# Optimization experiments

Measured on AMD Instinct MI355X. Metric: run time of the kernel, lower is better.

The kernel has to match this reference:

```python
import jax, jax.numpy as jnp
import numpy as np

OUT_FEATURES = 4096
IN_FEATURES = 4096
BATCH = 2048
NNZ = 1_600_000


def setup_inputs() -> dict:
    key = jax.random.key(0)
    k1, k2, k3, k4, k5 = jax.random.split(key, 5)
    rows = jax.random.randint(k1, (NNZ,), 0, OUT_FEATURES, dtype=jnp.int32)
    cols = jax.random.randint(k2, (NNZ,), 0, IN_FEATURES, dtype=jnp.int32)
    values = jax.random.normal(k3, (NNZ,), dtype=jnp.float32) * 0.02
    bias = jax.random.normal(k4, (OUT_FEATURES, 1), dtype=jnp.float32) * 0.02
    inp = jax.random.normal(k5, (IN_FEATURES, BATCH), dtype=jnp.float32)
    return {"inp": inp, "values": values, "bias": bias, "rows": rows, "cols": cols}


def reference(inp, values, bias, rows, cols):
    # Sparse COO addmm: out = bias + W @ inp, W sparse [OUT, IN].
    # Scatter-add the COO triplets into a dense weight (sums duplicates,
    # matching coalesced-COO spmm semantics), then one dense GEMM.
    W = jnp.zeros((OUT_FEATURES, IN_FEATURES), dtype=values.dtype).at[rows, cols].add(values)
    return W @ inp + bias  # [OUT, BATCH], bias [OUT,1] broadcasts over batch
```

## Files before the change

### kernel.cpp

```cpp
#include <hip/hip_runtime.h>
#include <stdint.h>

#define OUTF 4096
#define INF  4096
#define NBAT 2048
#define BM 128
#define BN 128
#define BK 32

typedef __attribute__((ext_vector_type(8))) short bf16x8;
typedef __attribute__((ext_vector_type(4))) float f32x4;
typedef __attribute__((ext_vector_type(4))) unsigned int u32x4;

typedef const __attribute__((address_space(1))) uint8_t* gptr_t;
typedef __attribute__((address_space(3))) uint8_t* lptr_t;

__device__ __forceinline__ uint32_t f2bf(float f) {
  uint32_t u = __builtin_bit_cast(uint32_t, f);
  return (u + 0x7FFFu + ((u >> 16) & 1u)) >> 16;
}

__global__ void zeroW_kernel(uint4* __restrict__ W) {
  W[(size_t)blockIdx.x * 256 + threadIdx.x] = make_uint4(0u, 0u, 0u, 0u);
}

__global__ void scatter_kernel(const float* __restrict__ vals,
                               const int* __restrict__ rows,
                               const int* __restrict__ cols,
                               float* __restrict__ W, int nnz) {
  int i = blockIdx.x * blockDim.x + threadIdx.x;
  if (i < nnz) atomicAdd(&W[(size_t)rows[i] * INF + cols[i]], vals[i]);
}

__global__ void packW_kernel(uint32_t* __restrict__ W) {
  size_t i = ((size_t)blockIdx.x * 256 + threadIdx.x) * 4;
  uint4 p = *(const uint4*)(W + i);
  uint32_t o[4];
  uint32_t w[4] = {p.x, p.y, p.z, p.w};
#pragma unroll
  for (int j = 0; j < 4; ++j) {
    float f = __builtin_bit_cast(float, w[j]);
    uint32_t hi = f2bf(f);
    float fhi = __builtin_bit_cast(float, hi << 16);
    uint32_t lo = f2bf(f - fhi);
    o[j] = (hi << 16) | lo;
  }
  *(uint4*)(W + i) = make_uint4(o[0], o[1], o[2], o[3]);
}

__global__ void packX_kernel(const float* __restrict__ X,
                             uint16_t* __restrict__ Xh,
                             uint16_t* __restrict__ Xl) {
  __shared__ float t[32][33];
  int n0 = blockIdx.x * 32, k0 = blockIdx.y * 32;
  int tx = threadIdx.x, ty = threadIdx.y;
#pragma unroll
  for (int j = 0; j < 4; ++j)
    t[ty + j * 8][tx] = X[(size_t)(k0 + ty + j * 8) * NBAT + n0 + tx];
  __syncthreads();
#pragma unroll
  for (int j = 0; j < 4; ++j) {
    int n = n0 + ty + j * 8, k = k0 + tx;
    float f = t[tx][ty + j * 8];
    uint32_t hi = f2bf(f);
    float fhi = __builtin_bit_cast(float, hi << 16);
    uint32_t lo = f2bf(f - fhi);
    Xh[(size_t)n * INF + k] = (uint16_t)hi;
    Xl[(size_t)n * INF + k] = (uint16_t)lo;
  }
}

__global__ __launch_bounds__(256, 2) void gemm_kernel(
    const uint32_t* __restrict__ Wp,
    const uint16_t* __restrict__ Xh,
    const uint16_t* __restrict__ Xl,
    const float* __restrict__ bias,
    float* __restrict__ out) {
  __shared__ __align__(16) uint8_t lds[32768];
  uint8_t* la = lds;
  uint8_t* lb = lds + 16384;

  const unsigned tid = threadIdx.x;
  const unsigned lane = tid & 63, wid = tid >> 6;
  const unsigned wr = wid >> 1, wc = wid & 1;

  unsigned newid = (blockIdx.x & 7) * 64 + (blockIdx.x >> 3);
  const unsigned bm = newid & 31, bn = newid >> 5;

  const uint8_t* aSrc[4];
  const uint8_t* bSrc[4];
#pragma unroll
  for (int i = 0; i < 4; ++i) {
    unsigned d = i * 4096 + tid * 16;
    unsigned row = d >> 7;
    unsigned ch = (d >> 4) & 7;
    unsigned sc = ch ^ (row & 7);
    aSrc[i] = (const uint8_t*)Wp + (size_t)(bm * BM + row) * (INF * 4) + sc * 16;
    const uint16_t* base = (sc & 4) ? Xl : Xh;
    bSrc[i] = (const uint8_t*)(base + (size_t)(bn * BN + row) * INF + (sc & 3) * 8);
  }

  const unsigned kg = lane >> 4, lr = lane & 15;
  unsigned aOff[4][2], bOffH[4], bOffL[4];
#pragma unroll
  for (int mi = 0; mi < 4; ++mi) {
    unsigned row = wr * 64 + mi * 16 + lr;
    aOff[mi][0] = row * 128 + (((kg * 2 + 0) ^ (row & 7)) * 16);
    aOff[mi][1] = row * 128 + (((kg * 2 + 1) ^ (row & 7)) * 16);
  }
#pragma unroll
  for (int ni = 0; ni < 4; ++ni) {
    unsigned col = wc * 64 + ni * 16 + lr;
    bOffH[ni] = col * 128 + (((0 + kg) ^ (col & 7)) * 16);
    bOffL[ni] = col * 128 + (((4 + kg) ^ (col & 7)) * 16);
  }

  f32x4 acc[4][4] = {};

  for (unsigned kt = 0; kt < INF / BK; ++kt) {
#pragma unroll
    for (int i = 0; i < 4; ++i) {
      __builtin_amdgcn_global_load_lds((gptr_t)(aSrc[i] + (size_t)kt * 128),
                                       (lptr_t)(la + i * 4096 + wid * 1024), 16, 0, 0);
      __builtin_amdgcn_global_load_lds((gptr_t)(bSrc[i] + (size_t)kt * 64),
                                       (lptr_t)(lb + i * 4096 + wid * 1024), 16, 0, 0);
    }
    __syncthreads();

    bf16x8 ah[4], al[4], bh[4], bl[4];
#pragma unroll
    for (int mi = 0; mi < 4; ++mi) {
      uint4 p0 = *(const uint4*)(la + aOff[mi][0]);
      uint4 p1 = *(const uint4*)(la + aOff[mi][1]);
      u32x4 h, l;
      h[0] = (p0.x >> 16) | (p0.y & 0xFFFF0000u);  l[0] = (p0.x & 0xFFFFu) | (p0.y << 16);
      h[1] = (p0.z >> 16) | (p0.w & 0xFFFF0000u);  l[1] = (p0.z & 0xFFFFu) | (p0.w << 16);
      h[2] = (p1.x >> 16) | (p1.y & 0xFFFF0000u);  l[2] = (p1.x & 0xFFFFu) | (p1.y << 16);
      h[3] = (p1.z >> 16) | (p1.w & 0xFFFF0000u);  l[3] = (p1.z & 0xFFFFu) | (p1.w << 16);
      ah[mi] = __builtin_bit_cast(bf16x8, h);
      al[mi] = __builtin_bit_cast(bf16x8, l);
    }
#pragma unroll
    for (int ni = 0; ni < 4; ++ni) {
      bh[ni] = *(const bf16x8*)(lb + bOffH[ni]);
      bl[ni] = *(const bf16x8*)(lb + bOffL[ni]);
    }
#pragma unroll
    for (int mi = 0; mi < 4; ++mi)
#pragma unroll
      for (int ni = 0; ni < 4; ++ni) {
        acc[mi][ni] = __builtin_amdgcn_mfma_f32_16x16x32_bf16(ah[mi], bh[ni], acc[mi][ni], 0, 0, 0);
        acc[mi][ni] = __builtin_amdgcn_mfma_f32_16x16x32_bf16(ah[mi], bl[ni], acc[mi][ni], 0, 0, 0);
        acc[mi][ni] = __builtin_amdgcn_mfma_f32_16x16x32_bf16(al[mi], bh[ni], acc[mi][ni], 0, 0, 0);
      }
    __syncthreads();
  }

  const unsigned lq = lane >> 4;
#pragma unroll
  for (int mi = 0; mi < 4; ++mi) {
    unsigned row0 = bm * BM + wr * 64 + mi * 16 + lq * 4;
#pragma unroll
    for (int ni = 0; ni < 4; ++ni) {
      unsigned col = bn * BN + wc * 64 + ni * 16 + lr;
#pragma unroll
      for (int r = 0; r < 4; ++r)
        out[(size_t)(row0 + r) * NBAT + col] = acc[mi][ni][r] + bias[row0 + r];
    }
  }
}

extern "C" void kernel_launch(void* const* d_in, const int* in_sizes, int n_in,
                              void* d_out, int out_size, void* d_ws, size_t ws_size,
                              hipStream_t stream) {
  const float* inp    = (const float*)d_in[0];
  const float* values = (const float*)d_in[1];
  const float* bias   = (const float*)d_in[2];
  const int*   rows   = (const int*)d_in[3];
  const int*   cols   = (const int*)d_in[4];
  const int nnz = in_sizes[1];
  float* out = (float*)d_out;

  uint8_t* ws = (uint8_t*)d_ws;
  float*    W  = (float*)ws;
  uint16_t* Xh = (uint16_t*)(ws + (64u << 20));
  uint16_t* Xl = (uint16_t*)(ws + (80u << 20));

  zeroW_kernel<<<(OUTF * (size_t)INF * 4) / (256 * 16), 256, 0, stream>>>((uint4*)W);
  scatter_kernel<<<(nnz + 255) / 256, 256, 0, stream>>>(values, rows, cols, W, nnz);
  packW_kernel<<<(OUTF * (size_t)INF / 4) / 256, 256, 0, stream>>>((uint32_t*)W);
  packX_kernel<<<dim3(NBAT / 32, INF / 32), dim3(32, 8), 0, stream>>>(inp, Xh, Xl);
  gemm_kernel<<<(OUTF / BM) * (NBAT / BN), 256, 0, stream>>>(
      (const uint32_t*)W, Xh, Xl, bias, out);
}
```

Baseline: 391.0 us.

## Fuse zero/packX, drop packW, split fp32 W in GEMM with pipelined split-K

Merges W zeroing and X packing into one launch and removes the separate W packing pass. The GEMM now reads raw fp32 W and splits it into bf16 hi/lo in registers. The GEMM moves to 128-thread blocks where two waves split K, with a double-buffered LDS pipeline, 32x32x16 MFMAs, and a reduction plus coalesced bias store through LDS. This removes a full 64MB read-write pass over W and kernel launch overhead, at the cost of more A-tile traffic and in-loop unpack ALU work. The lo part is now truncated instead of rounded, and there is only one block per CU.

Measured after the change: 1.390 ms. 3.55x slower.

```diff
diff --git a/kernel.cpp b/kernel.cpp
--- a/kernel.cpp
+++ b/kernel.cpp
@@ -4,14 +4,12 @@
 #define OUTF 4096
 #define INF  4096
 #define NBAT 2048
-#define BM 128
-#define BN 128
-#define BK 32
+#define T_STEPS 128
 
 typedef __attribute__((ext_vector_type(8))) short bf16x8;
+typedef __attribute__((ext_vector_type(16))) float f32x16;
 typedef __attribute__((ext_vector_type(4))) float f32x4;
 typedef __attribute__((ext_vector_type(4))) unsigned int u32x4;
-
 typedef const __attribute__((address_space(1))) uint8_t* gptr_t;
 typedef __attribute__((address_space(3))) uint8_t* lptr_t;
 
@@ -20,40 +18,28 @@
   return (u + 0x7FFFu + ((u >> 16) & 1u)) >> 16;
 }
 
-__global__ void zeroW_kernel(uint4* __restrict__ W) {
-  W[(size_t)blockIdx.x * 256 + threadIdx.x] = make_uint4(0u, 0u, 0u, 0u);
-}
-
-__global__ void scatter_kernel(const float* __restrict__ vals,
-                               const int* __restrict__ rows,
-                               const int* __restrict__ cols,
-                               float* __restrict__ W, int nnz) {
-  int i = blockIdx.x * blockDim.x + threadIdx.x;
-  if (i < nnz) atomicAdd(&W[(size_t)rows[i] * INF + cols[i]], vals[i]);
-}
-
-__global__ void packW_kernel(uint32_t* __restrict__ W) {
-  size_t i = ((size_t)blockIdx.x * 256 + threadIdx.x) * 4;
-  uint4 p = *(const uint4*)(W + i);
-  uint32_t o[4];
-  uint32_t w[4] = {p.x, p.y, p.z, p.w};
-#pragma unroll
-  for (int j = 0; j < 4; ++j) {
-    float f = __builtin_bit_cast(float, w[j]);
-    uint32_t hi = f2bf(f);
-    float fhi = __builtin_bit_cast(float, hi << 16);
-    uint32_t lo = f2bf(f - fhi);
-    o[j] = (hi << 16) | lo;
-  }
-  *(uint4*)(W + i) = make_uint4(o[0], o[1], o[2], o[3]);
-}
-
-__global__ void packX_kernel(const float* __restrict__ X,
-                             uint16_t* __restrict__ Xh,
-                             uint16_t* __restrict__ Xl) {
+__device__ __forceinline__ void split2(uint32_t u0, uint32_t u1,
+                                       uint32_t& h, uint32_t& l) {
+  uint32_t h0 = (u0 + 0x7FFFu + ((u0 >> 16) & 1u)) >> 16;
+  uint32_t h1 = (u1 + 0x7FFFu + ((u1 >> 16) & 1u)) >> 16;
+  float r0 = __builtin_bit_cast(float, u0) - __builtin_bit_cast(float, h0 << 16);
+  float r1 = __builtin_bit_cast(float, u1) - __builtin_bit_cast(float, h1 << 16);
+  h = h0 | (h1 << 16);
+  l = (__builtin_bit_cast(uint32_t, r0) >> 16) |
+      (__builtin_bit_cast(uint32_t, r1) & 0xFFFF0000u);
+}
+
+__global__ void zero_packX_kernel(uint4* __restrict__ W, const float* __restrict__ X,
+                                  uint16_t* __restrict__ Xh, uint16_t* __restrict__ Xl) {
+  unsigned bid = blockIdx.x;
+  if (bid < 16384) {
+    W[(size_t)bid * 256 + threadIdx.x] = make_uint4(0u, 0u, 0u, 0u);
+    return;
+  }
+  bid -= 16384;
   __shared__ float t[32][33];
-  int n0 = blockIdx.x * 32, k0 = blockIdx.y * 32;
-  int tx = threadIdx.x, ty = threadIdx.y;
+  int n0 = (bid & 63) * 32, k0 = (bid >> 6) * 32;
+  int tx = threadIdx.x & 31, ty = threadIdx.x >> 5;
 #pragma unroll
   for (int j = 0; j < 4; ++j)
     t[ty + j * 8][tx] = X[(size_t)(k0 + ty + j * 8) * NBAT + n0 + tx];
@@ -70,103 +56,161 @@
   }
 }
 
-__global__ __launch_bounds__(256, 2) void gemm_kernel(
-    const uint32_t* __restrict__ Wp,
-    const uint16_t* __restrict__ Xh,
-    const uint16_t* __restrict__ Xl,
-    const float* __restrict__ bias,
+__global__ void scatter_kernel(const float* __restrict__ vals,
+                               const int* __restrict__ rows,
+                               const int* __restrict__ cols,
+                               float* __restrict__ W, int nnz) {
+  int i = blockIdx.x * blockDim.x + threadIdx.x;
+  if (i < nnz) atomicAdd(&W[(size_t)rows[i] * INF + cols[i]], vals[i]);
+}
+
+#define WAIT_LGKM0 do { asm volatile("s_waitcnt lgkmcnt(0)" ::: "memory"); \
+                        __builtin_amdgcn_sched_barrier(0); } while (0)
+#define WAIT_VM(N)  asm volatile("s_waitcnt vmcnt(" #N ")" ::: "memory")
+#define BAR         __builtin_amdgcn_s_barrier()
+
+#define STAGE(BS) do { \
+  _Pragma("unroll") for (int j = 0; j < 8; ++j) \
+    __builtin_amdgcn_global_load_lds((gptr_t)(aPtr + j * 262144), \
+        (lptr_t)(lds + (BS) * 32768 + j * 2048 + kh * 1024), 16, 0, 0); \
+  _Pragma("unroll") for (int j = 0; j < 8; ++j) \
+    __builtin_amdgcn_global_load_lds((gptr_t)(bPtr + j * 131072), \
+        (lptr_t)(lds + (BS) * 32768 + 16384 + j * 2048 + kh * 1024), 16, 0, 0); \
+  aPtr += 64; bPtr += 32; \
+} while (0)
+
+#define READS(S, BO) do { \
+  _Pragma("unroll") for (int mi = 0; mi < 4; ++mi) { \
+    Ar##S[mi][0] = *(const uint4*)(lds + (BO) + aOff[mi][0]); \
+    Ar##S[mi][1] = *(const uint4*)(lds + (BO) + aOff[mi][1]); } \
+  _Pragma("unroll") for (int ni = 0; ni < 4; ++ni) { \
+    Bh##S[ni] = *(const bf16x8*)(lds + (BO) + 16384 + bOff[ni][0]); \
+    Bl##S[ni] = *(const bf16x8*)(lds + (BO) + 16384 + bOff[ni][1]); } \
+} while (0)
+
+#define UNPACK(S) do { \
+  _Pragma("unroll") for (int mi = 0; mi < 4; ++mi) { \
+    uint4 q0 = Ar##S[mi][0], q1 = Ar##S[mi][1]; \
+    u32x4 h, l; \
+    uint32_t th, tl; \
+    split2(q0.x, q0.y, th, tl); h[0] = th; l[0] = tl; \
+    split2(q0.z, q0.w, th, tl); h[1] = th; l[1] = tl; \
+    split2(q1.x, q1.y, th, tl); h[2] = th; l[2] = tl; \
+    split2(q1.z, q1.w, th, tl); h[3] = th; l[3] = tl; \
+    Ah##S[mi] = __builtin_bit_cast(bf16x8, h); \
+    Al##S[mi] = __builtin_bit_cast(bf16x8, l); } \
+} while (0)
+
+#define MFMAS(S) do { \
+  _Pragma("unroll") for (int mi = 0; mi < 4; ++mi) \
+  _Pragma("unroll") for (int ni = 0; ni < 4; ++ni) \
+    acc[mi][ni] = __builtin_amdgcn_mfma_f32_32x32x16_bf16(Ah##S[mi], Bh##S[ni], acc[mi][ni], 0, 0, 0); \
+  _Pragma("unroll") for (int mi = 0; mi < 4; ++mi) \
+  _Pragma("unroll") for (int ni = 0; ni < 4; ++ni) \
+    acc[mi][ni] = __builtin_amdgcn_mfma_f32_32x32x16_bf16(Ah##S[mi], Bl##S[ni], acc[mi][ni], 0, 0, 0); \
+  _Pragma("unroll") for (int mi = 0; mi < 4; ++mi) \
+  _Pragma("unroll") for (int ni = 0; ni < 4; ++ni) \
+    acc[mi][ni] = __builtin_amdgcn_mfma_f32_32x32x16_bf16(Al##S[mi], Bh##S[ni], acc[mi][ni], 0, 0, 0); \
+} while (0)
+
+#define STEP(C, N, t) do { \
+  if ((t) < 126) { STAGE((t) & 1); WAIT_VM(16); } \
+  else if ((t) == 126) { WAIT_VM(0); } \
+  if ((t) < 127) { BAR; READS(N, (((t) + 1) & 1) * 32768); } \
+  __builtin_amdgcn_s_setprio(1); MFMAS(C); __builtin_amdgcn_s_setprio(0); \
+  if ((t) < 127) { WAIT_LGKM0; UNPACK(N); BAR; } \
+} while (0)
+
+__global__ __launch_bounds__(128, 1) void gemm_kernel(
+    const uint32_t* __restrict__ Wp, const uint16_t* __restrict__ Xh,
+    const uint16_t* __restrict__ Xl, const float* __restrict__ bias,
     float* __restrict__ out) {
-  __shared__ __align__(16) uint8_t lds[32768];
-  uint8_t* la = lds;
-  uint8_t* lb = lds + 16384;
-
-  const unsigned tid = threadIdx.x;
-  const unsigned lane = tid & 63, wid = tid >> 6;
-  const unsigned wr = wid >> 1, wc = wid & 1;
+  __shared__ __align__(16) uint8_t lds[67584];
+  const unsigned tid = threadIdx.x, lane = tid & 63, kh = tid >> 6;
+  const unsigned ln31 = lane & 31, l5 = lane >> 5;
 
   unsigned newid = (blockIdx.x & 7) * 64 + (blockIdx.x >> 3);
   const unsigned bm = newid & 31, bn = newid >> 5;
 
-  const uint8_t* aSrc[4];
-  const uint8_t* bSrc[4];
-#pragma unroll
-  for (int i = 0; i < 4; ++i) {
-    unsigned d = i * 4096 + tid * 16;
-    unsigned row = d >> 7;
-    unsigned ch = (d >> 4) & 7;
-    unsigned sc = ch ^ (row & 7);
-    aSrc[i] = (const uint8_t*)Wp + (size_t)(bm * BM + row) * (INF * 4) + sc * 16;
-    const uint16_t* base = (sc & 4) ? Xl : Xh;
-    bSrc[i] = (const uint8_t*)(base + (size_t)(bn * BN + row) * INF + (sc & 3) * 8);
-  }
-
-  const unsigned kg = lane >> 4, lr = lane & 15;
-  unsigned aOff[4][2], bOffH[4], bOffL[4];
+  const unsigned tg = tid >> 3;
+  const unsigned sc = (tid & 7) ^ (tg & 7);
+  const uint8_t* aPtr = (const uint8_t*)Wp + (size_t)(bm * 128 + tg) * (INF * 4)
+                        + (sc >> 2) * (2048 * 4) + (sc & 3) * 16;
+  const uint16_t* xb = ((sc >> 1) & 1) ? Xl : Xh;
+  const uint8_t* bPtr = (const uint8_t*)xb + (size_t)(bn * 128 + tg) * (INF * 2)
+                        + (sc >> 2) * (2048 * 2) + (sc & 1) * 16;
+
+  unsigned aOff[4][2], bOff[4][2];
 #pragma unroll
   for (int mi = 0; mi < 4; ++mi) {
-    unsigned row = wr * 64 + mi * 16 + lr;
-    aOff[mi][0] = row * 128 + (((kg * 2 + 0) ^ (row & 7)) * 16);
-    aOff[mi][1] = row * 128 + (((kg * 2 + 1) ^ (row & 7)) * 16);
+    unsigned row = mi * 32 + ln31, x = row & 7, c0 = kh * 4 + l5 * 2;
+    aOff[mi][0] = row * 128 + ((c0 ^ x) << 4);
+    aOff[mi][1] = row * 128 + (((c0 + 1) ^ x) << 4);
   }
 #pragma unroll
   for (int ni = 0; ni < 4; ++ni) {
-    unsigned col = wc * 64 + ni * 16 + lr;
-    bOffH[ni] = col * 128 + (((0 + kg) ^ (col & 7)) * 16);
-    bOffL[ni] = col * 128 + (((4 + kg) ^ (col & 7)) * 16);
-  }
-
-  f32x4 acc[4][4] = {};
-
-  for (unsigned kt = 0; kt < INF / BK; ++kt) {
-#pragma unroll
-    for (int i = 0; i < 4; ++i) {
-      __builtin_amdgcn_global_load_lds((gptr_t)(aSrc[i] + (size_t)kt * 128),
-                                       (lptr_t)(la + i * 4096 + wid * 1024), 16, 0, 0);
-      __builtin_amdgcn_global_load_lds((gptr_t)(bSrc[i] + (size_t)kt * 64),
-                                       (lptr_t)(lb + i * 4096 + wid * 1024), 16, 0, 0);
-    }
-    __syncthreads();
-
-    bf16x8 ah[4], al[4], bh[4], bl[4];
-#pragma unroll
-    for (int mi = 0; mi < 4; ++mi) {
-      uint4 p0 = *(const uint4*)(la + aOff[mi][0]);
-      uint4 p1 = *(const uint4*)(la + aOff[mi][1]);
-      u32x4 h, l;
-      h[0] = (p0.x >> 16) | (p0.y & 0xFFFF0000u);  l[0] = (p0.x & 0xFFFFu) | (p0.y << 16);
-      h[1] = (p0.z >> 16) | (p0.w & 0xFFFF0000u);  l[1] = (p0.z & 0xFFFFu) | (p0.w << 16);
-      h[2] = (p1.x >> 16) | (p1.y & 0xFFFF0000u);  l[2] = (p1.x & 0xFFFFu) | (p1.y << 16);
-      h[3] = (p1.z >> 16) | (p1.w & 0xFFFF0000u);  l[3] = (p1.z & 0xFFFFu) | (p1.w << 16);
-      ah[mi] = __builtin_bit_cast(bf16x8, h);
-      al[mi] = __builtin_bit_cast(bf16x8, l);
-    }
-#pragma unroll
-    for (int ni = 0; ni < 4; ++ni) {
-      bh[ni] = *(const bf16x8*)(lb + bOffH[ni]);
-      bl[ni] = *(const bf16x8*)(lb + bOffL[ni]);
-    }
+    unsigned col = ni * 32 + ln31, x = col & 7;
+    bOff[ni][0] = col * 128 + (((kh * 4 + 0 + l5) ^ x) << 4);
+    bOff[ni][1] = col * 128 + (((kh * 4 + 2 + l5) ^ x) << 4);
+  }
+
+  f32x16 acc[4][4];
+#pragma unroll
+  for (int mi = 0; mi < 4; ++mi)
+#pragma unroll
+    for (int ni = 0; ni < 4; ++ni) acc[mi][ni] = (f32x16)(0.0f);
+
+  uint4 Ar0[4][2], Ar1[4][2];
+  bf16x8 Ah0[4], Al0[4], Bh0[4], Bl0[4];
+  bf16x8 Ah1[4], Al1[4], Bh1[4], Bl1[4];
+
+  STAGE(0);
+  STAGE(1);
+  WAIT_VM(16);
+  BAR;
+  READS(0, 0u);
+  WAIT_LGKM0;
+  UNPACK(0);
+
+  for (unsigned t = 0; t < T_STEPS; t += 2) {
+    STEP(0, 1, t);
+    STEP(1, 0, t + 1);
+  }
+
+  float* C = (float*)lds;
+  BAR;
+  if (kh == 0) {
 #pragma unroll
     for (int mi = 0; mi < 4; ++mi)
 #pragma unroll
-      for (int ni = 0; ni < 4; ++ni) {
-        acc[mi][ni] = __builtin_amdgcn_mfma_f32_16x16x32_bf16(ah[mi], bh[ni], acc[mi][ni], 0, 0, 0);
-        acc[mi][ni] = __builtin_amdgcn_mfma_f32_16x16x32_bf16(ah[mi], bl[ni], acc[mi][ni], 0, 0, 0);
-        acc[mi][ni] = __builtin_amdgcn_mfma_f32_16x16x32_bf16(al[mi], bh[ni], acc[mi][ni], 0, 0, 0);
-      }
-    __syncthreads();
-  }
-
-  const unsigned lq = lane >> 4;
-#pragma unroll
-  for (int mi = 0; mi < 4; ++mi) {
-    unsigned row0 = bm * BM + wr * 64 + mi * 16 + lq * 4;
-#pragma unroll
-    for (int ni = 0; ni < 4; ++ni) {
-      unsigned col = bn * BN + wc * 64 + ni * 16 + lr;
-#pragma unroll
-      for (int r = 0; r < 4; ++r)
-        out[(size_t)(row0 + r) * NBAT + col] = acc[mi][ni][r] + bias[row0 + r];
-    }
+      for (int ni = 0; ni < 4; ++ni)
+#pragma unroll
+        for (int r = 0; r < 16; ++r) {
+          unsigned row = mi * 32 + (r & 3) + 8 * (r >> 2) + 4 * l5;
+          C[row * 132 + ni * 32 + ln31] = acc[mi][ni][r];
+        }
+  }
+  BAR;
+  if (kh == 1) {
+#pragma unroll
+    for (int mi = 0; mi < 4; ++mi)
+#pragma unroll
+      for (int ni = 0; ni < 4; ++ni)
+#pragma unroll
+        for (int r = 0; r < 16; ++r) {
+          unsigned row = mi * 32 + (r & 3) + 8 * (r >> 2) + 4 * l5;
+          C[row * 132 + ni * 32 + ln31] += acc[mi][ni][r];
+        }
+  }
+  BAR;
+#pragma unroll 4
+  for (unsigned it = 0; it < 32; ++it) {
+    unsigned idx = it * 128 + tid;
+    unsigned row = idx >> 5, c4 = idx & 31;
+    f32x4 v = *(const f32x4*)(C + row * 132 + c4 * 4);
+    float b = bias[bm * 128 + row];
+    v[0] += b; v[1] += b; v[2] += b; v[3] += b;
+    *(f32x4*)(out + (size_t)(bm * 128 + row) * NBAT + bn * 128 + c4 * 4) = v;
   }
 }
 
@@ -186,10 +230,7 @@
   uint16_t* Xh = (uint16_t*)(ws + (64u << 20));
   uint16_t* Xl = (uint16_t*)(ws + (80u << 20));
 
-  zeroW_kernel<<<(OUTF * (size_t)INF * 4) / (256 * 16), 256, 0, stream>>>((uint4*)W);
+  zero_packX_kernel<<<16384 + 8192, 256, 0, stream>>>((uint4*)W, inp, Xh, Xl);
   scatter_kernel<<<(nnz + 255) / 256, 256, 0, stream>>>(values, rows, cols, W, nnz);
-  packW_kernel<<<(OUTF * (size_t)INF / 4) / 256, 256, 0, stream>>>((uint32_t*)W);
-  packX_kernel<<<dim3(NBAT / 32, INF / 32), dim3(32, 8), 0, stream>>>(inp, Xh, Xl);
-  gemm_kernel<<<(OUTF / BM) * (NBAT / BN), 256, 0, stream>>>(
-      (const uint32_t*)W, Xh, Xl, bias, out);
-}
+  gemm_kernel<<<512, 128, 0, stream>>>((const uint32_t*)W, Xh, Xl, bias, out);
+}
```
